# Kernel tuning notes

Measured on AMD Instinct MI355X. Metric: run time of the kernel, lower is better.

Reference implementation:

```python
import jax, jax.numpy as jnp
import numpy as np

B, S, C = 4, 2048, 768
H = 6
D = C // H  # head_dim = 128


def setup_inputs() -> dict:
    key = jax.random.key(0)
    k_x, k_wa, k_ba, k_wp, k_bp = jax.random.split(key, 5)
    scale = 1.0 / np.sqrt(C)
    return {
        "x": jax.random.normal(k_x, (B, S, C), dtype=jnp.float32),
        "w_attn": jax.random.normal(k_wa, (C, 3 * C), dtype=jnp.float32) * scale,
        "b_attn": jax.random.normal(k_ba, (3 * C,), dtype=jnp.float32) * 0.02,
        "w_proj": jax.random.normal(k_wp, (C, C), dtype=jnp.float32) * scale,
        "b_proj": jax.random.normal(k_bp, (C,), dtype=jnp.float32) * 0.02,
    }


def reference(x, w_attn, b_attn, w_proj, b_proj):
    Bb, Ss, Cc = x.shape
    qkv = x @ w_attn + b_attn                      # [B,S,3C]
    q, k, v = jnp.split(qkv, 3, axis=-1)
    # [B,S,C] -> [B,H,S,D]
    q = q.reshape(Bb, Ss, H, D).transpose(0, 2, 1, 3)
    k = k.reshape(Bb, Ss, H, D).transpose(0, 2, 1, 3)
    v = v.reshape(Bb, Ss, H, D).transpose(0, 2, 1, 3)
    scores = jnp.einsum("bhsd,bhtd->bhst", q, k) / jnp.sqrt(jnp.float32(D))
    causal = jnp.tril(jnp.ones((Ss, Ss), dtype=bool))  # [S,S]
    scores = jnp.where(causal[None, None], scores, -jnp.inf)
    attn = jax.nn.softmax(scores, axis=-1)             # [B,H,S,S]
    out = jnp.einsum("bhst,bhtd->bhsd", attn, v)       # [B,H,S,D]
    out = out.transpose(0, 2, 1, 3).reshape(Bb, Ss, Cc)
    return out @ w_proj + b_proj
```

## Files before the change

kernel.cpp:

```cpp
#include <hip/hip_runtime.h>
#include <hip/hip_bf16.h>
#include <stdint.h>

#define SS 2048
#define CC 768
#define C3 2304
#define NITEMS (32 * 24)

typedef float f32x4 __attribute__((ext_vector_type(4)));
typedef short s16x8 __attribute__((ext_vector_type(8)));

__device__ __forceinline__ unsigned short f2bf(float f) {
  union { float f; unsigned int u; } v; v.f = f;
  unsigned int r = (v.u + 0x7FFFu + ((v.u >> 16) & 1u)) >> 16;
  return (unsigned short)r;
}

__device__ __forceinline__ s16x8 ld8(const unsigned short* p) {
  return *reinterpret_cast<const s16x8*>(p);
}

__device__ __forceinline__ unsigned int cvt_pk_bf16(float lo, float hi) {
  unsigned int r;
  asm("v_cvt_pk_bf16_f32 %0, %1, %2" : "=v"(r) : "v"(lo), "v"(hi));
  return r;
}

__device__ __forceinline__ void gload_lds16(const unsigned short* g, unsigned short* l) {
  __builtin_amdgcn_global_load_lds(
      (const __attribute__((address_space(1))) void*)g,
      (__attribute__((address_space(3))) void*)l, 16, 0, 0);
}

__global__ __launch_bounds__(256) void cast_bf16_kernel(
    const float* __restrict__ src, unsigned short* __restrict__ dst, int n4) {
  int i = blockIdx.x * 256 + threadIdx.x;
  if (i < n4) {
    float4 v = reinterpret_cast<const float4*>(src)[i];
    ushort4 o;
    o.x = f2bf(v.x); o.y = f2bf(v.y); o.z = f2bf(v.z); o.w = f2bf(v.w);
    reinterpret_cast<ushort4*>(dst)[i] = o;
  }
}

__global__ __launch_bounds__(256) void transpose_cast_kernel(
    const float* __restrict__ src, unsigned short* __restrict__ dst, int R, int C) {
  __shared__ float tile[32][33];
  int c0 = blockIdx.x * 32, r0 = blockIdx.y * 32;
  int tx = threadIdx.x & 31, ty = threadIdx.x >> 5;
  #pragma unroll
  for (int i = 0; i < 32; i += 8)
    tile[ty + i][tx] = src[(size_t)(r0 + ty + i) * C + c0 + tx];
  __syncthreads();
  #pragma unroll
  for (int i = 0; i < 32; i += 8)
    dst[(size_t)(c0 + ty + i) * R + r0 + tx] = f2bf(tile[tx][ty + i]);
}

__global__ __launch_bounds__(256) void vtrans_kernel(
    const unsigned short* __restrict__ qkv, unsigned short* __restrict__ vT) {
  __shared__ unsigned short t[64 * 128];
  const int tid = threadIdx.x;
  const int n0 = blockIdx.x * 64;
  const int bh = blockIdx.y;
  const int b = bh / 6, h = bh % 6;
  #pragma unroll
  for (int it = 0; it < 4; ++it) {
    int c = it * 256 + tid;
    int n = c >> 4, slot = c & 15;
    s16x8 v = ld8(qkv + (size_t)(b * SS + n0 + n) * C3 + 2 * CC + h * 128 + slot * 8);
    int ss = slot ^ ((n >> 3) & 7);
    *reinterpret_cast<s16x8*>(&t[n * 128 + ss * 8]) = v;
  }
  __syncthreads();
  #pragma unroll
  for (int it = 0; it < 4; ++it) {
    int c = it * 256 + tid;
    int d = c >> 3, n8 = (c & 7) * 8;
    s16x8 o;
    #pragma unroll
    for (int j = 0; j < 8; ++j) {
      int n = n8 + j;
      int sl = (d >> 3) ^ ((n >> 3) & 7);
      o[j] = (short)t[n * 128 + sl * 8 + (d & 7)];
    }
    *reinterpret_cast<s16x8*>(&vT[((size_t)bh * 128 + d) * SS + n0 + n8]) = o;
  }
}

template <int OUT_BF16>
__global__ __launch_bounds__(256) void gemm_lds_kernel(
    const unsigned short* __restrict__ A, const unsigned short* __restrict__ Bt,
    const float* __restrict__ bias, void* __restrict__ out, int M, int N, int K) {
  __shared__ unsigned short lA[2][128 * 32];
  __shared__ unsigned short lB[2][128 * 32];
  const int tid = threadIdx.x, lane = tid & 63, w = tid >> 6;
  const int nbx = gridDim.x;
  int bid = blockIdx.y * nbx + blockIdx.x;
  const int cpx = (nbx * gridDim.y) >> 3;
  bid = (bid & 7) * cpx + (bid >> 3);
  const int m0 = (bid / nbx) * 128, n0 = (bid % nbx) * 128;
  const int lm = lane & 15, lg = lane >> 4;
  const int wm = (w >> 1) * 64, wn = (w & 1) * 64;
  const int sr = lane >> 2;
  const int ssl = ((lane & 3) ^ ((sr >> 1) & 3)) * 8;
  int aOff[4], bOff[4];
  #pragma unroll
  for (int i = 0; i < 4; ++i) {
    int ra = wm + i * 16 + lm, rb = wn + i * 16 + lm;
    aOff[i] = ra * 32 + ((lg ^ ((ra >> 1) & 3)) * 8);
    bOff[i] = rb * 32 + ((lg ^ ((rb >> 1) & 3)) * 8);
  }
  f32x4 acc[4][4] = {};
  const int nt = K / 32;
  #define GSTAGE(tt, bb)                                                      \
    {                                                                         \
      const int k0_ = (tt) * 32;                                              \
      _Pragma("unroll")                                                       \
      for (int i_ = 0; i_ < 2; ++i_) {                                        \
        int c_ = w * 2 + i_;                                                  \
        int row_ = c_ * 16 + sr;                                              \
        gload_lds16(A + (size_t)(m0 + row_) * K + k0_ + ssl, &lA[bb][c_ * 512]); \
        gload_lds16(Bt + (size_t)(n0 + row_) * K + k0_ + ssl, &lB[bb][c_ * 512]); \
      }                                                                       \
    }
  GSTAGE(0, 0);
  #pragma unroll 1
  for (int t = 0; t < nt; ++t) {
    if (t + 1 < nt) {
      GSTAGE(t + 1, (t + 1) & 1);
      asm volatile("s_waitcnt vmcnt(4)" ::: "memory");
    } else {
      asm volatile("s_waitcnt vmcnt(0)" ::: "memory");
    }
    __builtin_amdgcn_sched_barrier(0);
    __builtin_amdgcn_s_barrier();
    const int cu = t & 1;
    s16x8 af[4], bf[4];
    #pragma unroll
    for (int i = 0; i < 4; ++i) af[i] = ld8(&lA[cu][aOff[i]]);
    #pragma unroll
    for (int i = 0; i < 4; ++i) bf[i] = ld8(&lB[cu][bOff[i]]);
    __builtin_amdgcn_s_setprio(1);
    #pragma unroll
    for (int mi = 0; mi < 4; ++mi)
      #pragma unroll
      for (int ni = 0; ni < 4; ++ni)
        acc[mi][ni] = __builtin_amdgcn_mfma_f32_16x16x32_bf16(af[mi], bf[ni], acc[mi][ni], 0, 0, 0);
    __builtin_amdgcn_s_setprio(0);
    asm volatile("s_waitcnt lgkmcnt(0)" ::: "memory");
    __builtin_amdgcn_sched_barrier(0);
    __builtin_amdgcn_s_barrier();
  }
  #pragma unroll
  for (int mi = 0; mi < 4; ++mi) {
    #pragma unroll
    for (int ni = 0; ni < 4; ++ni) {
      const int row = m0 + wm + mi * 16 + lg * 4;
      const int col = n0 + wn + ni * 16 + lm;
      const float bs = bias[col];
      #pragma unroll
      for (int r = 0; r < 4; ++r) {
        float v = acc[mi][ni][r] + bs;
        if (OUT_BF16)
          ((unsigned short*)out)[(size_t)(row + r) * N + col] = f2bf(v);
        else
          ((float*)out)[(size_t)(row + r) * N + col] = v;
      }
    }
  }
  #undef GSTAGE
}

__global__ __launch_bounds__(256) void attn_kernel(
    const unsigned short* __restrict__ qkv,
    const unsigned short* __restrict__ vT,
    unsigned short* __restrict__ aout,
    int* __restrict__ ctr) {
  const int tid = threadIdx.x, lane = tid & 63, w = tid >> 6;
  const int lm = lane & 15, lg = lane >> 4;
  __shared__ unsigned short kbuf[2][64 * 128];
  __shared__ unsigned short vbuf[2][128 * 64];
  __shared__ unsigned int pb[4][16 * 44];
  __shared__ int s_item;
  const float scale = 0.08838834764831845f;
  unsigned int* pr = &pb[w][lm * 44];
  const int klg4 = lane >> 4, ks16 = lane & 15;
  const int vlg8 = lane >> 3, vs8 = lane & 7;
  for (;;) {
    __syncthreads();
    if (tid == 0) s_item = atomicAdd(ctr, 1);
    __syncthreads();
    const int item = s_item;
    if (item >= NITEMS) return;
    const int qt = 31 - (item / 24);
    const int bh = item % 24;
    const int b = bh / 6, h = bh % 6;
    const int q0 = qt * 64, wq0 = q0 + w * 16;
    const unsigned short* base = qkv + (size_t)b * SS * C3;
    const unsigned short* kg = base + CC + h * 128;
    const unsigned short* vg = vT + (size_t)bh * 128 * SS;
    s16x8 qf[4];
    {
      const unsigned short* qp = base + (size_t)(wq0 + lm) * C3 + h * 128 + lg * 8;
      #pragma unroll
      for (int ks = 0; ks < 4; ++ks) qf[ks] = ld8(qp + ks * 32);
    }
    #define ASTAGE(tt, bb)                                                    \
      {                                                                       \
        const int n1_ = (tt) * 64;                                            \
        _Pragma("unroll")                                                     \
        for (int i_ = 0; i_ < 4; ++i_) {                                      \
          int c_ = w * 4 + i_;                                                \
          int r_ = c_ * 4 + klg4;                                             \
          gload_lds16(kg + (size_t)(n1_ + r_) * C3 + ((ks16 ^ (r_ & 7)) * 8), \
                      &kbuf[bb][c_ * 512]);                                   \
        }                                                                     \
        _Pragma("unroll")                                                     \
        for (int i_ = 0; i_ < 4; ++i_) {                                      \
          int c_ = w * 4 + i_;                                                \
          int d_ = c_ * 8 + vlg8;                                             \
          gload_lds16(vg + (size_t)d_ * SS + n1_ + ((vs8 ^ vlg8) * 8),        \
                      &vbuf[bb][c_ * 512]);                                   \
        }                                                                     \
      }
    f32x4 oacc[8] = {};
    float m_run = -1e30f, l_run = 0.0f;
    const int nt = qt + 1;
    ASTAGE(0, 0);
    #pragma unroll 1
    for (int t = 0; t < nt; ++t) {
      if (t + 1 < nt) {
        ASTAGE(t + 1, (t + 1) & 1);
        asm volatile("s_waitcnt vmcnt(8)" ::: "memory");
      } else {
        asm volatile("s_waitcnt vmcnt(0)" ::: "memory");
      }
      __builtin_amdgcn_sched_barrier(0);
      __builtin_amdgcn_s_barrier();
      const int n0 = t * 64;
      const int cu = t & 1;
      const unsigned short* kb = kbuf[cu];
      const unsigned short* vb = vbuf[cu];
      f32x4 sacc[4] = {};
      __builtin_amdgcn_s_setprio(1);
      #pragma unroll
      for (int nsub = 0; nsub < 4; ++nsub) {
        const int kr = (nsub * 16 + lm) * 128;
        #pragma unroll
        for (int ks = 0; ks < 4; ++ks) {
          s16x8 kf = ld8(&kb[kr + (((ks * 4 + lg) ^ (lm & 7)) * 8)]);
          sacc[nsub] = __builtin_amdgcn_mfma_f32_16x16x32_bf16(kf, qf[ks], sacc[nsub], 0, 0, 0);
        }
      }
      __builtin_amdgcn_s_setprio(0);
      const int qg = wq0 + lm;
      const bool full = (n0 + 63 <= wq0);
      float xs[4][4];
      float tmax = -1e30f;
      #pragma unroll
      for (int nsub = 0; nsub < 4; ++nsub) {
        #pragma unroll
        for (int r = 0; r < 4; ++r) {
          int n = n0 + nsub * 16 + lg * 4 + r;
          float x = sacc[nsub][r] * scale;
          if (!full && n > qg) x = -1e30f;
          xs[nsub][r] = x;
          tmax = fmaxf(tmax, x);
        }
      }
      tmax = fmaxf(tmax, __shfl_xor(tmax, 16));
      tmax = fmaxf(tmax, __shfl_xor(tmax, 32));
      const bool noresc = __all(tmax - m_run <= 8.0f);
      const float m_new = noresc ? m_run : fmaxf(m_run, tmax);
      float psum = 0.0f;
      unsigned int pk_[4][2];
      #pragma unroll
      for (int nsub = 0; nsub < 4; ++nsub) {
        float p0 = __expf(xs[nsub][0] - m_new);
        float p1 = __expf(xs[nsub][1] - m_new);
        float p2 = __expf(xs[nsub][2] - m_new);
        float p3 = __expf(xs[nsub][3] - m_new);
        psum += (p0 + p1) + (p2 + p3);
        pk_[nsub][0] = cvt_pk_bf16(p0, p1);
        pk_[nsub][1] = cvt_pk_bf16(p2, p3);
      }
      psum += __shfl_xor(psum, 16);
      psum += __shfl_xor(psum, 32);
      if (!noresc) {
        const float resc = __expf(m_run - m_new);
        l_run *= resc;
        m_run = m_new;
        float rs[4];
        #pragma unroll
        for (int r = 0; r < 4; ++r) rs[r] = __shfl(resc, lg * 4 + r);
        #pragma unroll
        for (int dsub = 0; dsub < 8; ++dsub)
          #pragma unroll
          for (int r = 0; r < 4; ++r) oacc[dsub][r] *= rs[r];
      }
      l_run += psum;
      #pragma unroll
      for (int nsub = 0; nsub < 4; ++nsub) {
        uint2 pk2; pk2.x = pk_[nsub][0]; pk2.y = pk_[nsub][1];
        *reinterpret_cast<uint2*>(&pr[nsub * 8 + lg * 2]) = pk2;
      }
      __builtin_amdgcn_s_setprio(1);
      #pragma unroll
      for (int nch = 0; nch < 2; ++nch) {
        s16x8 pf = *reinterpret_cast<const s16x8*>(&pr[nch * 16 + lg * 4]);
        #pragma unroll
        for (int dsub = 0; dsub < 8; ++dsub) {
          const int vr = (dsub * 16 + lm) * 64;
          s16x8 vf = ld8(&vb[vr + (((nch * 4 + lg) ^ (lm & 7)) * 8)]);
          oacc[dsub] = __builtin_amdgcn_mfma_f32_16x16x32_bf16(pf, vf, oacc[dsub], 0, 0, 0);
        }
      }
      __builtin_amdgcn_s_setprio(0);
      asm volatile("s_waitcnt lgkmcnt(0)" ::: "memory");
      __builtin_amdgcn_sched_barrier(0);
      __builtin_amdgcn_s_barrier();
    }
    #undef ASTAGE
    float linv[4];
    #pragma unroll
    for (int r = 0; r < 4; ++r) linv[r] = 1.0f / __shfl(l_run, lg * 4 + r);
    #pragma unroll
    for (int dsub = 0; dsub < 8; ++dsub) {
      const int col = h * 128 + dsub * 16 + lm;
      #pragma unroll
      for (int r = 0; r < 4; ++r)
        aout[(size_t)(b * SS + wq0 + lg * 4 + r) * CC + col] =
            f2bf(oacc[dsub][r] * linv[r]);
    }
  }
}

extern "C" void kernel_launch(void* const* d_in, const int* in_sizes, int n_in,
                              void* d_out, int out_size, void* d_ws, size_t ws_size,
                              hipStream_t stream) {
  const float* x      = (const float*)d_in[0];
  const float* w_attn = (const float*)d_in[1];
  const float* b_attn = (const float*)d_in[2];
  const float* w_proj = (const float*)d_in[3];
  const float* b_proj = (const float*)d_in[4];
  float* out = (float*)d_out;

  const size_t M = 4 * (size_t)SS;
  unsigned short* ws = (unsigned short*)d_ws;
  unsigned short* xb   = ws;
  unsigned short* waT  = xb + M * CC;
  unsigned short* wpT  = waT + (size_t)C3 * CC;
  unsigned short* qkv  = wpT + (size_t)CC * CC;
  unsigned short* aout = qkv + M * C3;
  unsigned short* vT   = xb;
  int* ctr = (int*)(aout + M * CC);

  int n4 = (int)(M * CC / 4);
  cast_bf16_kernel<<<(n4 + 255) / 256, 256, 0, stream>>>(x, xb, n4);
  transpose_cast_kernel<<<dim3(C3 / 32, CC / 32), 256, 0, stream>>>(w_attn, waT, CC, C3);
  transpose_cast_kernel<<<dim3(CC / 32, CC / 32), 256, 0, stream>>>(w_proj, wpT, CC, CC);

  gemm_lds_kernel<1><<<dim3(C3 / 128, M / 128), 256, 0, stream>>>(
      xb, waT, b_attn, (void*)qkv, (int)M, C3, CC);

  vtrans_kernel<<<dim3(SS / 64, 24), 256, 0, stream>>>(qkv, vT);

  hipMemsetAsync(ctr, 0, sizeof(int), stream);
  attn_kernel<<<512, 256, 0, stream>>>(qkv, vT, aout, ctr);

  gemm_lds_kernel<0><<<dim3(CC / 128, M / 128), 256, 0, stream>>>(
      aout, wpT, b_proj, (void*)out, (int)M, CC, CC);
}
```

Measured before the change: 158.1 us.

## Shrink attention blocks to 2 waves, single-buffer K/V, fold softmax scale into Q weights

The attention kernel now uses 128-thread blocks covering 32 query rows, with twice as many work items and grid blocks, and single-buffered K and V LDS tiles. K for the next tile is prefetched after QK^T and V after PV, with separate barriers between them. This cuts LDS use per block and raises occupancy and load balance. The 1/sqrt(D) scale is folded into the Q columns of the transposed QKV weight and bias, removing a multiply per score, at the cost of more barriers and less prefetch lead time.

```diff
diff --git a/kernel.cpp b/kernel.cpp
--- a/kernel.cpp
+++ b/kernel.cpp
@@ -5,7 +5,8 @@
 #define SS 2048
 #define CC 768
 #define C3 2304
-#define NITEMS (32 * 24)
+#define NITEMS (64 * 24)
+#define QSC 0.08838834764831845f
 
 typedef float f32x4 __attribute__((ext_vector_type(4)));
 typedef short s16x8 __attribute__((ext_vector_type(8)));
@@ -44,7 +45,8 @@
 }
 
 __global__ __launch_bounds__(256) void transpose_cast_kernel(
-    const float* __restrict__ src, unsigned short* __restrict__ dst, int R, int C) {
+    const float* __restrict__ src, unsigned short* __restrict__ dst, int R, int C,
+    int nsc) {
   __shared__ float tile[32][33];
   int c0 = blockIdx.x * 32, r0 = blockIdx.y * 32;
   int tx = threadIdx.x & 31, ty = threadIdx.x >> 5;
@@ -53,8 +55,12 @@
     tile[ty + i][tx] = src[(size_t)(r0 + ty + i) * C + c0 + tx];
   __syncthreads();
   #pragma unroll
-  for (int i = 0; i < 32; i += 8)
-    dst[(size_t)(c0 + ty + i) * R + r0 + tx] = f2bf(tile[tx][ty + i]);
+  for (int i = 0; i < 32; i += 8) {
+    int oc = c0 + ty + i;
+    float v = tile[tx][ty + i];
+    if (oc < nsc) v *= QSC;
+    dst[(size_t)oc * R + r0 + tx] = f2bf(v);
+  }
 }
 
 __global__ __launch_bounds__(256) void vtrans_kernel(
@@ -91,7 +97,8 @@
 template <int OUT_BF16>
 __global__ __launch_bounds__(256) void gemm_lds_kernel(
     const unsigned short* __restrict__ A, const unsigned short* __restrict__ Bt,
-    const float* __restrict__ bias, void* __restrict__ out, int M, int N, int K) {
+    const float* __restrict__ bias, void* __restrict__ out, int M, int N, int K,
+    int nsc) {
   __shared__ unsigned short lA[2][128 * 32];
   __shared__ unsigned short lB[2][128 * 32];
   const int tid = threadIdx.x, lane = tid & 63, w = tid >> 6;
@@ -158,7 +165,8 @@
     for (int ni = 0; ni < 4; ++ni) {
       const int row = m0 + wm + mi * 16 + lg * 4;
       const int col = n0 + wn + ni * 16 + lm;
-      const float bs = bias[col];
+      float bs = bias[col];
+      if (col < nsc) bs *= QSC;
       #pragma unroll
       for (int r = 0; r < 4; ++r) {
         float v = acc[mi][ni][r] + bs;
@@ -172,19 +180,18 @@
   #undef GSTAGE
 }
 
-__global__ __launch_bounds__(256) void attn_kernel(
+__global__ __launch_bounds__(128) void attn_kernel(
     const unsigned short* __restrict__ qkv,
     const unsigned short* __restrict__ vT,
     unsigned short* __restrict__ aout,
     int* __restrict__ ctr) {
   const int tid = threadIdx.x, lane = tid & 63, w = tid >> 6;
   const int lm = lane & 15, lg = lane >> 4;
-  __shared__ unsigned short kbuf[2][64 * 128];
-  __shared__ unsigned short vbuf[2][128 * 64];
-  __shared__ unsigned int pb[4][16 * 44];
+  __shared__ unsigned short kbuf[64 * 128];
+  __shared__ unsigned short vbuf[128 * 64];
+  __shared__ unsigned int pb[2][16 * 36];
   __shared__ int s_item;
-  const float scale = 0.08838834764831845f;
-  unsigned int* pr = &pb[w][lm * 44];
+  unsigned int* pr = &pb[w][lm * 36];
   const int klg4 = lane >> 4, ks16 = lane & 15;
   const int vlg8 = lane >> 3, vs8 = lane & 7;
   for (;;) {
@@ -193,10 +200,10 @@
     __syncthreads();
     const int item = s_item;
     if (item >= NITEMS) return;
-    const int qt = 31 - (item / 24);
+    const int qt = 63 - (item / 24);
     const int bh = item % 24;
     const int b = bh / 6, h = bh % 6;
-    const int q0 = qt * 64, wq0 = q0 + w * 16;
+    const int wq0 = qt * 32 + w * 16;
     const unsigned short* base = qkv + (size_t)b * SS * C3;
     const unsigned short* kg = base + CC + h * 128;
     const unsigned short* vg = vT + (size_t)bh * 128 * SS;
@@ -206,42 +213,39 @@
       #pragma unroll
       for (int ks = 0; ks < 4; ++ks) qf[ks] = ld8(qp + ks * 32);
     }
-    #define ASTAGE(tt, bb)                                                    \
+    #define AK(tt)                                                            \
       {                                                                       \
         const int n1_ = (tt) * 64;                                            \
         _Pragma("unroll")                                                     \
-        for (int i_ = 0; i_ < 4; ++i_) {                                      \
-          int c_ = w * 4 + i_;                                                \
+        for (int i_ = 0; i_ < 8; ++i_) {                                      \
+          int c_ = w * 8 + i_;                                                \
           int r_ = c_ * 4 + klg4;                                             \
           gload_lds16(kg + (size_t)(n1_ + r_) * C3 + ((ks16 ^ (r_ & 7)) * 8), \
-                      &kbuf[bb][c_ * 512]);                                   \
+                      &kbuf[c_ * 512]);                                       \
         }                                                                     \
+      }
+    #define AV(tt)                                                            \
+      {                                                                       \
+        const int n1_ = (tt) * 64;                                            \
         _Pragma("unroll")                                                     \
-        for (int i_ = 0; i_ < 4; ++i_) {                                      \
-          int c_ = w * 4 + i_;                                                \
+        for (int i_ = 0; i_ < 8; ++i_) {                                      \
+          int c_ = w * 8 + i_;                                                \
           int d_ = c_ * 8 + vlg8;                                             \
-          gload_lds16(vg + (size_t)d_ * SS + n1_ + ((vs8 ^ vlg8) * 8),        \
-                      &vbuf[bb][c_ * 512]);                                   \
+          gload_lds16(vg + (size_t)d_ * SS + n1_ + ((vs8 ^ (d_ & 7)) * 8),    \
+                      &vbuf[c_ * 512]);                                       \
         }                                                                     \
       }
     f32x4 oacc[8] = {};
     float m_run = -1e30f, l_run = 0.0f;
-    const int nt = qt + 1;
-    ASTAGE(0, 0);
+    const int nt = (qt >> 1) + 1;
+    AK(0);
+    AV(0);
     #pragma unroll 1
     for (int t = 0; t < nt; ++t) {
-      if (t + 1 < nt) {
-        ASTAGE(t + 1, (t + 1) & 1);
-        asm volatile("s_waitcnt vmcnt(8)" ::: "memory");
-      } else {
-        asm volatile("s_waitcnt vmcnt(0)" ::: "memory");
-      }
+      asm volatile("s_waitcnt vmcnt(8)" ::: "memory");
       __builtin_amdgcn_sched_barrier(0);
       __builtin_amdgcn_s_barrier();
       const int n0 = t * 64;
-      const int cu = t & 1;
-      const unsigned short* kb = kbuf[cu];
-      const unsigned short* vb = vbuf[cu];
       f32x4 sacc[4] = {};
       __builtin_amdgcn_s_setprio(1);
       #pragma unroll
@@ -249,11 +253,15 @@
         const int kr = (nsub * 16 + lm) * 128;
         #pragma unroll
         for (int ks = 0; ks < 4; ++ks) {
-          s16x8 kf = ld8(&kb[kr + (((ks * 4 + lg) ^ (lm & 7)) * 8)]);
+          s16x8 kf = ld8(&kbuf[kr + (((ks * 4 + lg) ^ (lm & 7)) * 8)]);
           sacc[nsub] = __builtin_amdgcn_mfma_f32_16x16x32_bf16(kf, qf[ks], sacc[nsub], 0, 0, 0);
         }
       }
       __builtin_amdgcn_s_setprio(0);
+      asm volatile("s_waitcnt lgkmcnt(0)" ::: "memory");
+      __builtin_amdgcn_sched_barrier(0);
+      __builtin_amdgcn_s_barrier();
+      if (t + 1 < nt) AK(t + 1);
       const int qg = wq0 + lm;
       const bool full = (n0 + 63 <= wq0);
       float xs[4][4];
@@ -263,7 +271,7 @@
         #pragma unroll
         for (int r = 0; r < 4; ++r) {
           int n = n0 + nsub * 16 + lg * 4 + r;
-          float x = sacc[nsub][r] * scale;
+          float x = sacc[nsub][r];
           if (!full && n > qg) x = -1e30f;
           xs[nsub][r] = x;
           tmax = fmaxf(tmax, x);
@@ -305,6 +313,13 @@
         uint2 pk2; pk2.x = pk_[nsub][0]; pk2.y = pk_[nsub][1];
         *reinterpret_cast<uint2*>(&pr[nsub * 8 + lg * 2]) = pk2;
       }
+      if (t + 1 < nt) {
+        asm volatile("s_waitcnt vmcnt(8)" ::: "memory");
+      } else {
+        asm volatile("s_waitcnt vmcnt(0)" ::: "memory");
+      }
+      __builtin_amdgcn_sched_barrier(0);
+      __builtin_amdgcn_s_barrier();
       __builtin_amdgcn_s_setprio(1);
       #pragma unroll
       for (int nch = 0; nch < 2; ++nch) {
@@ -312,7 +327,7 @@
         #pragma unroll
         for (int dsub = 0; dsub < 8; ++dsub) {
           const int vr = (dsub * 16 + lm) * 64;
-          s16x8 vf = ld8(&vb[vr + (((nch * 4 + lg) ^ (lm & 7)) * 8)]);
+          s16x8 vf = ld8(&vbuf[vr + (((nch * 4 + lg) ^ (lm & 7)) * 8)]);
           oacc[dsub] = __builtin_amdgcn_mfma_f32_16x16x32_bf16(pf, vf, oacc[dsub], 0, 0, 0);
         }
       }
@@ -320,8 +335,10 @@
       asm volatile("s_waitcnt lgkmcnt(0)" ::: "memory");
       __builtin_amdgcn_sched_barrier(0);
       __builtin_amdgcn_s_barrier();
-    }
-    #undef ASTAGE
+      if (t + 1 < nt) AV(t + 1);
+    }
+    #undef AK
+    #undef AV
     float linv[4];
     #pragma unroll
     for (int r = 0; r < 4; ++r) linv[r] = 1.0f / __shfl(l_run, lg * 4 + r);
@@ -358,17 +375,17 @@
 
   int n4 = (int)(M * CC / 4);
   cast_bf16_kernel<<<(n4 + 255) / 256, 256, 0, stream>>>(x, xb, n4);
-  transpose_cast_kernel<<<dim3(C3 / 32, CC / 32), 256, 0, stream>>>(w_attn, waT, CC, C3);
-  transpose_cast_kernel<<<dim3(CC / 32, CC / 32), 256, 0, stream>>>(w_proj, wpT, CC, CC);
+  transpose_cast_kernel<<<dim3(C3 / 32, CC / 32), 256, 0, stream>>>(w_attn, waT, CC, C3, CC);
+  transpose_cast_kernel<<<dim3(CC / 32, CC / 32), 256, 0, stream>>>(w_proj, wpT, CC, CC, 0);
 
   gemm_lds_kernel<1><<<dim3(C3 / 128, M / 128), 256, 0, stream>>>(
-      xb, waT, b_attn, (void*)qkv, (int)M, C3, CC);
+      xb, waT, b_attn, (void*)qkv, (int)M, C3, CC, CC);
 
   vtrans_kernel<<<dim3(SS / 64, 24), 256, 0, stream>>>(qkv, vT);
 
   hipMemsetAsync(ctr, 0, sizeof(int), stream);
-  attn_kernel<<<512, 256, 0, stream>>>(qkv, vT, aout, ctr);
+  attn_kernel<<<1024, 128, 0, stream>>>(qkv, vT, aout, ctr);
 
   gemm_lds_kernel<0><<<dim3(CC / 128, M / 128), 256, 0, stream>>>(
-      aout, wpT, b_proj, (void*)out, (int)M, CC, CC);
-}
+      aout, wpT, b_proj, (void*)out, (int)M, CC, CC, 0);
+}
```

New measurement: 173.4 us. +9.7%, slower.

## Triple-buffer GEMM LDS pipeline and fold attention scale into Q weights

Applied to the files above, without the earlier changes.

The GEMM's global-to-LDS staging goes from double to triple buffering, prefetching two K-tiles ahead with adjusted vmcnt waits, to hide more memory latency. The 1/sqrt(D) softmax scale is folded into the Q columns of the transposed QKV weight and its bias, which removes a per-score multiply in the attention kernel. Triple buffering raises LDS use per block and may reduce occupancy. The V-load swizzle expression is rewritten in an equivalent form.

```diff
diff --git a/kernel.cpp b/kernel.cpp
--- a/kernel.cpp
+++ b/kernel.cpp
@@ -6,6 +6,7 @@
 #define CC 768
 #define C3 2304
 #define NITEMS (32 * 24)
+#define QSC 0.08838834764831845f
 
 typedef float f32x4 __attribute__((ext_vector_type(4)));
 typedef short s16x8 __attribute__((ext_vector_type(8)));
@@ -44,7 +45,8 @@
 }
 
 __global__ __launch_bounds__(256) void transpose_cast_kernel(
-    const float* __restrict__ src, unsigned short* __restrict__ dst, int R, int C) {
+    const float* __restrict__ src, unsigned short* __restrict__ dst, int R, int C,
+    int nsc) {
   __shared__ float tile[32][33];
   int c0 = blockIdx.x * 32, r0 = blockIdx.y * 32;
   int tx = threadIdx.x & 31, ty = threadIdx.x >> 5;
@@ -53,8 +55,12 @@
     tile[ty + i][tx] = src[(size_t)(r0 + ty + i) * C + c0 + tx];
   __syncthreads();
   #pragma unroll
-  for (int i = 0; i < 32; i += 8)
-    dst[(size_t)(c0 + ty + i) * R + r0 + tx] = f2bf(tile[tx][ty + i]);
+  for (int i = 0; i < 32; i += 8) {
+    int oc = c0 + ty + i;
+    float v = tile[tx][ty + i];
+    if (oc < nsc) v *= QSC;
+    dst[(size_t)oc * R + r0 + tx] = f2bf(v);
+  }
 }
 
 __global__ __launch_bounds__(256) void vtrans_kernel(
@@ -91,9 +97,10 @@
 template <int OUT_BF16>
 __global__ __launch_bounds__(256) void gemm_lds_kernel(
     const unsigned short* __restrict__ A, const unsigned short* __restrict__ Bt,
-    const float* __restrict__ bias, void* __restrict__ out, int M, int N, int K) {
-  __shared__ unsigned short lA[2][128 * 32];
-  __shared__ unsigned short lB[2][128 * 32];
+    const float* __restrict__ bias, void* __restrict__ out, int M, int N, int K,
+    int nsc) {
+  __shared__ unsigned short lA[3][128 * 32];
+  __shared__ unsigned short lB[3][128 * 32];
   const int tid = threadIdx.x, lane = tid & 63, w = tid >> 6;
   const int nbx = gridDim.x;
   int bid = blockIdx.y * nbx + blockIdx.x;
@@ -125,17 +132,20 @@
       }                                                                       \
     }
   GSTAGE(0, 0);
+  if (nt > 1) GSTAGE(1, 1);
   #pragma unroll 1
   for (int t = 0; t < nt; ++t) {
-    if (t + 1 < nt) {
-      GSTAGE(t + 1, (t + 1) & 1);
+    if (t + 2 < nt) {
+      GSTAGE(t + 2, (t + 2) % 3);
+      asm volatile("s_waitcnt vmcnt(8)" ::: "memory");
+    } else if (t + 1 < nt) {
       asm volatile("s_waitcnt vmcnt(4)" ::: "memory");
     } else {
       asm volatile("s_waitcnt vmcnt(0)" ::: "memory");
     }
     __builtin_amdgcn_sched_barrier(0);
     __builtin_amdgcn_s_barrier();
-    const int cu = t & 1;
+    const int cu = t % 3;
     s16x8 af[4], bf[4];
     #pragma unroll
     for (int i = 0; i < 4; ++i) af[i] = ld8(&lA[cu][aOff[i]]);
@@ -158,7 +168,8 @@
     for (int ni = 0; ni < 4; ++ni) {
       const int row = m0 + wm + mi * 16 + lg * 4;
       const int col = n0 + wn + ni * 16 + lm;
-      const float bs = bias[col];
+      float bs = bias[col];
+      if (col < nsc) bs *= QSC;
       #pragma unroll
       for (int r = 0; r < 4; ++r) {
         float v = acc[mi][ni][r] + bs;
@@ -183,7 +194,6 @@
   __shared__ unsigned short vbuf[2][128 * 64];
   __shared__ unsigned int pb[4][16 * 44];
   __shared__ int s_item;
-  const float scale = 0.08838834764831845f;
   unsigned int* pr = &pb[w][lm * 44];
   const int klg4 = lane >> 4, ks16 = lane & 15;
   const int vlg8 = lane >> 3, vs8 = lane & 7;
@@ -220,7 +230,7 @@
         for (int i_ = 0; i_ < 4; ++i_) {                                      \
           int c_ = w * 4 + i_;                                                \
           int d_ = c_ * 8 + vlg8;                                             \
-          gload_lds16(vg + (size_t)d_ * SS + n1_ + ((vs8 ^ vlg8) * 8),        \
+          gload_lds16(vg + (size_t)d_ * SS + n1_ + ((vs8 ^ (d_ & 7)) * 8),    \
                       &vbuf[bb][c_ * 512]);                                   \
         }                                                                     \
       }
@@ -263,7 +273,7 @@
         #pragma unroll
         for (int r = 0; r < 4; ++r) {
           int n = n0 + nsub * 16 + lg * 4 + r;
-          float x = sacc[nsub][r] * scale;
+          float x = sacc[nsub][r];
           if (!full && n > qg) x = -1e30f;
           xs[nsub][r] = x;
           tmax = fmaxf(tmax, x);
@@ -358,11 +368,11 @@
 
   int n4 = (int)(M * CC / 4);
   cast_bf16_kernel<<<(n4 + 255) / 256, 256, 0, stream>>>(x, xb, n4);
-  transpose_cast_kernel<<<dim3(C3 / 32, CC / 32), 256, 0, stream>>>(w_attn, waT, CC, C3);
-  transpose_cast_kernel<<<dim3(CC / 32, CC / 32), 256, 0, stream>>>(w_proj, wpT, CC, CC);
+  transpose_cast_kernel<<<dim3(C3 / 32, CC / 32), 256, 0, stream>>>(w_attn, waT, CC, C3, CC);
+  transpose_cast_kernel<<<dim3(CC / 32, CC / 32), 256, 0, stream>>>(w_proj, wpT, CC, CC, 0);
 
   gemm_lds_kernel<1><<<dim3(C3 / 128, M / 128), 256, 0, stream>>>(
-      xb, waT, b_attn, (void*)qkv, (int)M, C3, CC);
+      xb, waT, b_attn, (void*)qkv, (int)M, C3, CC, CC);
 
   vtrans_kernel<<<dim3(SS / 64, 24), 256, 0, stream>>>(qkv, vT);
 
@@ -370,5 +380,5 @@
   attn_kernel<<<512, 256, 0, stream>>>(qkv, vT, aout, ctr);
 
   gemm_lds_kernel<0><<<dim3(CC / 128, M / 128), 256, 0, stream>>>(
-      aout, wpT, b_proj, (void*)out, (int)M, CC, CC);
-}
+      aout, wpT, b_proj, (void*)out, (int)M, CC, CC, 0);
+}
```

After: 159.2 us. Within noise of the previous version (+0.7%).
